# Kernel tuning notes

Hardware: AMD Instinct MI355X
Metric: run time of the kernel (lower is better)

## Reference

```python
import jax, jax.numpy as jnp
import numpy as np

K = 32  # num_neighbors in DynamicRadiusChannelFusion


def _sqdist(p):
    # p: (B, N, 3) -> pairwise squared distances (B, N, N)
    n2 = jnp.sum(p * p, axis=-1)
    d = n2[:, :, None] + n2[:, None, :] - 2.0 * jnp.einsum('bnd,bmd->bnm', p, p)
    return d


def _fuse(x, feats, W, b):
    # KNN on xyz coords (first 3 channels), gather neighbor feats,
    # relative edge features -> linear -> ReLU -> max over neighbors.
    d = _sqdist(x[..., :3])                      # (B, N, N)
    _, idx = jax.lax.top_k(-d, K)                # (B, N, K) int32
    nbr = jax.vmap(lambda f, i: f[i])(feats, idx)  # (B, N, K, C) gather
    rel = nbr - feats[:, :, None, :]             # edge features
    msg = jax.nn.relu(jnp.einsum('bnkc,cd->bnkd', rel, W) + b)
    return jnp.max(msg, axis=2), idx             # (B, N, C), (B, N, K)


def setup_inputs() -> dict:
    key = jax.random.key(0)
    ks = jax.random.split(key, 14)
    B, N, D, C, NC = 4, 8000, 9, 64, 13
    s = lambda *sh: 1.0 / np.sqrt(sh[0])
    return {
        'x': jax.random.normal(ks[0], (B, N, D), jnp.float32),
        'enc_w1': jax.random.normal(ks[1], (D, C), jnp.float32) * s(D),
        'enc_b1': jnp.zeros((C,), jnp.float32),
        'enc_w2': jax.random.normal(ks[2], (C, C), jnp.float32) * s(C),
        'enc_b2': jnp.zeros((C,), jnp.float32),
        'f1_w': jax.random.normal(ks[3], (C, C), jnp.float32) * s(C),
        'f1_b': jnp.zeros((C,), jnp.float32),
        'f2_w': jax.random.normal(ks[4], (C, C), jnp.float32) * s(C),
        'f2_b': jnp.zeros((C,), jnp.float32),
        'cls_w1': jax.random.normal(ks[5], (C, C // 2), jnp.float32) * s(C),
        'cls_b1': jnp.zeros((C // 2,), jnp.float32),
        'cls_w2': jax.random.normal(ks[6], (C // 2, NC), jnp.float32) * s(C // 2),
        'cls_b2': jnp.zeros((NC,), jnp.float32),
    }


def reference(x, enc_w1, enc_b1, enc_w2, enc_b2, f1_w, f1_b, f2_w, f2_b,
              cls_w1, cls_b1, cls_w2, cls_b2):
    # encoder: Linear -> ReLU -> Linear
    feats = jax.nn.relu(x @ enc_w1 + enc_b1) @ enc_w2 + enc_b2  # (B, N, 64)
    out1, _ = _fuse(x, feats, f1_w, f1_b)
    out2, _ = _fuse(x, feats, f2_w, f2_b)
    fused = out1 + out2
    # classifier: Linear -> ReLU -> Linear
    logits = jax.nn.relu(fused @ cls_w1 + cls_b1) @ cls_w2 + cls_b2
    return logits  # (B, N, num_classes)
```

## Files before the change

kernel.cpp:

```cpp
#include <hip/hip_runtime.h>
#include <stdint.h>

#define NPTS 8000
#define NBATCH 4
#define TOTALP (NBATCH * NPTS)
#define KSEL 32
#define QPB 64
#define SPLIT 4
#define CPW (NPTS / SPLIT)
#define PDEPTH 16

typedef uint32_t u32;
typedef unsigned long long u64;

__global__ __launch_bounds__(256) void encode_kernel(
    const float* __restrict__ x,
    const float* __restrict__ ew1, const float* __restrict__ eb1,
    const float* __restrict__ ew2, const float* __restrict__ eb2,
    const float* __restrict__ f1w, const float* __restrict__ f2w,
    float* __restrict__ g1, float* __restrict__ g2,
    float4* __restrict__ cand)
{
    __shared__ float sw1[9 * 64];
    __shared__ float sw2[64 * 64];
    __shared__ float sf1[64 * 64];
    __shared__ float sf2[64 * 64];
    __shared__ float sb1[64];
    __shared__ float sb2[64];
    __shared__ float shb[4][64];
    __shared__ float sfb[4][64];

    const int tid = threadIdx.x;
    for (int i = tid; i < 9 * 64; i += 256) sw1[i] = ew1[i];
    for (int i = tid; i < 64 * 64; i += 256) {
        sw2[i] = ew2[i]; sf1[i] = f1w[i]; sf2[i] = f2w[i];
    }
    if (tid < 64) { sb1[tid] = eb1[tid]; sb2[tid] = eb2[tid]; }
    __syncthreads();

    const int lane = tid & 63;
    const int w = tid >> 6;
    const int gw = blockIdx.x * 4 + w;
    const int nw = 256 * 4;

    #pragma unroll 1
    for (int it = 0; it < 32; ++it) {
        int p = gw + it * nw;
        int pc = p < TOTALP ? p : TOTALP - 1;
        const float* xp = x + (size_t)pc * 9;

        float acc = sb1[lane];
        #pragma unroll
        for (int i = 0; i < 9; ++i) acc = fmaf(xp[i], sw1[i * 64 + lane], acc);
        shb[w][lane] = fmaxf(acc, 0.f);
        __syncthreads();

        float fa = sb2[lane];
        #pragma unroll
        for (int c = 0; c < 64; ++c) fa = fmaf(shb[w][c], sw2[c * 64 + lane], fa);
        sfb[w][lane] = fa;
        __syncthreads();

        float a1 = 0.f, a2 = 0.f;
        #pragma unroll
        for (int c = 0; c < 64; ++c) {
            float fv = sfb[w][c];
            a1 = fmaf(fv, sf1[c * 64 + lane], a1);
            a2 = fmaf(fv, sf2[c * 64 + lane], a2);
        }
        if (p < TOTALP) {
            g1[(size_t)p * 64 + lane] = a1;
            g2[(size_t)p * 64 + lane] = a2;
            if (lane == 0) {
                float cx = xp[0], cy = xp[1], cz = xp[2];
                float n2 = __fadd_rn(__fadd_rn(__fmul_rn(cx, cx),
                                               __fmul_rn(cy, cy)),
                                     __fmul_rn(cz, cz));
                cand[p] = make_float4(cx, cy, cz, n2);
            }
        }
        __syncthreads();
    }
}

__global__ __launch_bounds__(256) void knn_scan_kernel(
    const float4* __restrict__ cand, int* __restrict__ idxo)
{
    __shared__ u64 smem[4096];
    const int b = blockIdx.y;
    const int lane = threadIdx.x & 63;
    const int w = threadIdx.x >> 6;
    const int q = blockIdx.x * QPB + lane;
    const float4* cb = cand + (size_t)b * NPTS;

    const float4 qv = cb[q];
    const float qx = qv.x, qy = qv.y, qz = qv.z, qn2 = qv.w;

    u64 sk[KSEL];
    #pragma unroll
    for (int i = 0; i < KSEL; ++i) sk[i] = ~0ULL;
    u64 thr = ~0ULL;
    int c = 0;
    u64* pend = smem + w * (PDEPTH * 64);

#define DRAINB()                                                          \
    do {                                                                  \
        u64 p[PDEPTH];                                                    \
        _Pragma("unroll")                                                 \
        for (int j = 0; j < PDEPTH; ++j) p[j] = pend[j * 64 + lane];      \
        _Pragma("unroll")                                                 \
        for (int j = 0; j < PDEPTH; ++j) p[j] = (j < c) ? p[j] : ~0ULL;   \
        _Pragma("unroll")                                                 \
        for (int k = 2; k <= PDEPTH; k <<= 1) {                           \
            _Pragma("unroll")                                             \
            for (int j = k >> 1; j > 0; j >>= 1) {                        \
                _Pragma("unroll")                                         \
                for (int i = 0; i < PDEPTH; ++i) {                        \
                    if ((i & j) == 0) {                                   \
                        const int ip = i | j;                             \
                        const bool asc = ((i & k) == 0);                  \
                        u64 a = p[i], bb = p[ip];                         \
                        u64 lo = a < bb ? a : bb;                         \
                        u64 hi = a < bb ? bb : a;                         \
                        p[i]  = asc ? lo : hi;                            \
                        p[ip] = asc ? hi : lo;                            \
                    }                                                     \
                }                                                         \
            }                                                             \
        }                                                                 \
        _Pragma("unroll")                                                 \
        for (int j = 0; j < PDEPTH; ++j) {                                \
            u64 a = sk[16 + j], bb = p[PDEPTH - 1 - j];                   \
            sk[16 + j] = a < bb ? a : bb;                                 \
        }                                                                 \
        _Pragma("unroll")                                                 \
        for (int dd = 16; dd > 0; dd >>= 1) {                             \
            _Pragma("unroll")                                             \
            for (int i = 0; i < KSEL; ++i) {                              \
                if ((i & dd) == 0) {                                      \
                    const int ip = i | dd;                                \
                    u64 a = sk[i], bb = sk[ip];                           \
                    sk[i]  = a < bb ? a : bb;                             \
                    sk[ip] = a < bb ? bb : a;                             \
                }                                                         \
            }                                                             \
        }                                                                 \
        c = 0;                                                            \
        thr = sk[KSEL - 1];                                               \
    } while (0)

#define PROC(cv, ci_)                                                     \
    do {                                                                  \
        float dot_ = fmaf(qz, (cv).z, fmaf(qy, (cv).y, __fmul_rn(qx, (cv).x))); \
        float d_ = __fsub_rn(__fadd_rn(qn2, (cv).w), __fmul_rn(2.0f, dot_)); \
        d_ = fmaxf(d_, 0.0f);   \
        u64 key_ = (((u64)__float_as_uint(d_)) << 13) | (u64)(ci_);       \
        bool take_ = key_ < thr;                                          \
        pend[(size_t)c * 64 + lane] = key_;                               \
        c += (int)take_;                                                  \
    } while (0)

    const int c0 = w * CPW;
    #pragma unroll 1
    for (int i = 0; i < CPW; i += 4) {
        const int ci = c0 + i;
        float4 cv0 = cb[ci + 0];
        float4 cv1 = cb[ci + 1];
        float4 cv2 = cb[ci + 2];
        float4 cv3 = cb[ci + 3];
        PROC(cv0, ci + 0);
        PROC(cv1, ci + 1);
        PROC(cv2, ci + 2);
        PROC(cv3, ci + 3);
        if (__any(c >= PDEPTH - 3)) DRAINB();
    }
    DRAINB();
#undef PROC
#undef DRAINB

#define MERGE32(kidx)                                                     \
    do {                                                                  \
        u64 o[KSEL];                                                      \
        _Pragma("unroll")                                                 \
        for (int t = 0; t < KSEL; ++t)                                    \
            o[t] = smem[(kidx) * 2048 + t * 64 + lane];                   \
        _Pragma("unroll")                                                 \
        for (int i = 0; i < KSEL; ++i) {                                  \
            u64 a = sk[i], bb = o[KSEL - 1 - i];                          \
            sk[i] = a < bb ? a : bb;                                      \
        }                                                                 \
        _Pragma("unroll")                                                 \
        for (int dd = 16; dd > 0; dd >>= 1) {                             \
            _Pragma("unroll")                                             \
            for (int i = 0; i < KSEL; ++i) {                              \
                if ((i & dd) == 0) {                                      \
                    const int ip = i | dd;                                \
                    u64 a = sk[i], bb = sk[ip];                           \
                    sk[i]  = a < bb ? a : bb;                             \
                    sk[ip] = a < bb ? bb : a;                             \
                }                                                         \
            }                                                             \
        }                                                                 \
    } while (0)

    __syncthreads();
    if (w == 1) {
        #pragma unroll
        for (int t = 0; t < KSEL; ++t) smem[t * 64 + lane] = sk[t];
    }
    if (w == 3) {
        #pragma unroll
        for (int t = 0; t < KSEL; ++t) smem[2048 + t * 64 + lane] = sk[t];
    }
    __syncthreads();
    if (w == 0) MERGE32(0);
    if (w == 2) MERGE32(1);
    __syncthreads();
    if (w == 2) {
        #pragma unroll
        for (int t = 0; t < KSEL; ++t) smem[t * 64 + lane] = sk[t];
    }
    __syncthreads();
    if (w == 0) {
        MERGE32(0);
        int* op = idxo + ((size_t)b * NPTS + q) * KSEL;
        #pragma unroll
        for (int i = 0; i < KSEL; ++i) op[i] = (int)(sk[i] & 0x1FFFULL);
    }
#undef MERGE32
}

__global__ __launch_bounds__(256) void fuse_kernel(
    const float* __restrict__ g1, const float* __restrict__ g2,
    const int* __restrict__ idxo,
    const float* __restrict__ f1b, const float* __restrict__ f2b,
    float* __restrict__ fused)
{
    const int lane = threadIdx.x & 63;
    const int gw = (int)((blockIdx.x * 256 + threadIdx.x) >> 6);
    const int nw = 512 * 4;
    const float bias1 = f1b[lane];
    const float bias2 = f2b[lane];
    for (int p = gw; p < TOTALP; p += nw) {
        int b = p / NPTS;
        const int* mi = idxo + (size_t)p * KSEL;
        const float* G1 = g1 + (size_t)b * NPTS * 64;
        const float* G2 = g2 + (size_t)b * NPTS * 64;
        float base1 = bias1 - g1[(size_t)p * 64 + lane];
        float base2 = bias2 - g2[(size_t)p * 64 + lane];
        float a1 = 0.f, a2 = 0.f;
        #pragma unroll
        for (int k = 0; k < KSEL; ++k) {
            int j = mi[k];
            a1 = fmaxf(a1, G1[(size_t)j * 64 + lane] + base1);
            a2 = fmaxf(a2, G2[(size_t)j * 64 + lane] + base2);
        }
        fused[(size_t)p * 64 + lane] = a1 + a2;
    }
}

__global__ __launch_bounds__(256) void cls_kernel(
    const float* __restrict__ fused,
    const float* __restrict__ cw1, const float* __restrict__ cb1,
    const float* __restrict__ cw2, const float* __restrict__ cb2,
    float* __restrict__ out)
{
    __shared__ float sw1[64 * 32];
    __shared__ float sw2[32 * 13];
    __shared__ float sb1[32];
    __shared__ float sb2[13];
    const int tid = threadIdx.x;
    for (int i = tid; i < 64 * 32; i += 256) sw1[i] = cw1[i];
    for (int i = tid; i < 32 * 13; i += 256) sw2[i] = cw2[i];
    if (tid < 32) sb1[tid] = cb1[tid];
    if (tid < 13) sb2[tid] = cb2[tid];
    __syncthreads();

    int p = blockIdx.x * 256 + tid;
    if (p >= TOTALP) return;

    float fu[64];
    const float4* fp = (const float4*)(fused + (size_t)p * 64);
    #pragma unroll
    for (int i = 0; i < 16; ++i) {
        float4 v = fp[i];
        fu[i * 4 + 0] = v.x; fu[i * 4 + 1] = v.y;
        fu[i * 4 + 2] = v.z; fu[i * 4 + 3] = v.w;
    }
    float h[32];
    #pragma unroll
    for (int j = 0; j < 32; j += 4) {
        float ax = sb1[j], ay = sb1[j + 1], az = sb1[j + 2], aw = sb1[j + 3];
        #pragma unroll
        for (int c = 0; c < 64; ++c) {
            float4 wv = *(const float4*)&sw1[c * 32 + j];
            ax = fmaf(fu[c], wv.x, ax);
            ay = fmaf(fu[c], wv.y, ay);
            az = fmaf(fu[c], wv.z, az);
            aw = fmaf(fu[c], wv.w, aw);
        }
        h[j] = fmaxf(ax, 0.f); h[j + 1] = fmaxf(ay, 0.f);
        h[j + 2] = fmaxf(az, 0.f); h[j + 3] = fmaxf(aw, 0.f);
    }
    float* op = out + (size_t)p * 13;
    #pragma unroll
    for (int o = 0; o < 13; ++o) {
        float acc = sb2[o];
        #pragma unroll
        for (int j = 0; j < 32; ++j) acc = fmaf(h[j], sw2[j * 13 + o], acc);
        op[o] = acc;
    }
}

extern "C" void kernel_launch(void* const* d_in, const int* in_sizes, int n_in,
                              void* d_out, int out_size, void* d_ws, size_t ws_size,
                              hipStream_t stream)
{
    const float* x   = (const float*)d_in[0];
    const float* ew1 = (const float*)d_in[1];
    const float* eb1 = (const float*)d_in[2];
    const float* ew2 = (const float*)d_in[3];
    const float* eb2 = (const float*)d_in[4];
    const float* f1w = (const float*)d_in[5];
    const float* f1b = (const float*)d_in[6];
    const float* f2w = (const float*)d_in[7];
    const float* f2b = (const float*)d_in[8];
    const float* cw1 = (const float*)d_in[9];
    const float* cb1 = (const float*)d_in[10];
    const float* cw2 = (const float*)d_in[11];
    const float* cb2 = (const float*)d_in[12];
    float* out = (float*)d_out;

    float*  g1    = (float*)d_ws;
    float*  g2    = g1 + (size_t)TOTALP * 64;
    float4* cand  = (float4*)(g2 + (size_t)TOTALP * 64);
    int*    idxo  = (int*)(cand + (size_t)TOTALP);
    float*  fused = (float*)(idxo + (size_t)TOTALP * KSEL);

    hipLaunchKernelGGL(encode_kernel, dim3(256), dim3(256), 0, stream,
                       x, ew1, eb1, ew2, eb2, f1w, f2w, g1, g2, cand);
    hipLaunchKernelGGL(knn_scan_kernel, dim3(125, NBATCH), dim3(256), 0, stream,
                       cand, idxo);
    hipLaunchKernelGGL(fuse_kernel, dim3(512), dim3(256), 0, stream,
                       g1, g2, idxo, f1b, f2b, fused);
    hipLaunchKernelGGL(cls_kernel, dim3(125), dim3(256), 0, stream,
                       fused, cw1, cb1, cw2, cb2, out);
}
```

Measured before the change: 524.1 us.

## Split KNN candidate scan across two block groups with a merge kernel

Splits the KNN candidate range into two halves handled by separate block groups, doubling the grid from 500 to 1000 blocks. The partial top-32 lists are written out and merged in a new bitonic-merge kernel that stores indices in k-major layout. The encoder moves from block-wide barriers to wave-local syncs with contiguous per-wave point chunks. The fuse kernel moves to a per-batch grid that reads the transposed index layout. The extra merge kernel and partial-key traffic add memory cost in exchange for more parallelism in the dominant scan.

```diff
diff --git a/kernel.cpp b/kernel.cpp
--- a/kernel.cpp
+++ b/kernel.cpp
@@ -7,7 +7,8 @@
 #define KSEL 32
 #define QPB 64
 #define SPLIT 4
-#define CPW (NPTS / SPLIT)
+#define CSPLIT 2
+#define CPW (NPTS / (CSPLIT * SPLIT))
 #define PDEPTH 16
 
 typedef uint32_t u32;
@@ -40,26 +41,30 @@
 
     const int lane = tid & 63;
     const int w = tid >> 6;
-    const int gw = blockIdx.x * 4 + w;
-    const int nw = 256 * 4;
+    const int wave_id = blockIdx.x * 4 + w;
+
+#define WSYNC() do { \
+        asm volatile("s_waitcnt lgkmcnt(0)" ::: "memory"); \
+        __builtin_amdgcn_wave_barrier(); \
+    } while (0)
 
     #pragma unroll 1
-    for (int it = 0; it < 32; ++it) {
-        int p = gw + it * nw;
-        int pc = p < TOTALP ? p : TOTALP - 1;
-        const float* xp = x + (size_t)pc * 9;
+    for (int it = 0; it < 16; ++it) {
+        const int p = wave_id * 16 + it;
+        const float* xp = x + (size_t)p * 9;
 
         float acc = sb1[lane];
         #pragma unroll
         for (int i = 0; i < 9; ++i) acc = fmaf(xp[i], sw1[i * 64 + lane], acc);
         shb[w][lane] = fmaxf(acc, 0.f);
-        __syncthreads();
+        WSYNC();
 
         float fa = sb2[lane];
         #pragma unroll
         for (int c = 0; c < 64; ++c) fa = fmaf(shb[w][c], sw2[c * 64 + lane], fa);
+        WSYNC();
         sfb[w][lane] = fa;
-        __syncthreads();
+        WSYNC();
 
         float a1 = 0.f, a2 = 0.f;
         #pragma unroll
@@ -68,26 +73,26 @@
             a1 = fmaf(fv, sf1[c * 64 + lane], a1);
             a2 = fmaf(fv, sf2[c * 64 + lane], a2);
         }
-        if (p < TOTALP) {
-            g1[(size_t)p * 64 + lane] = a1;
-            g2[(size_t)p * 64 + lane] = a2;
-            if (lane == 0) {
-                float cx = xp[0], cy = xp[1], cz = xp[2];
-                float n2 = __fadd_rn(__fadd_rn(__fmul_rn(cx, cx),
-                                               __fmul_rn(cy, cy)),
-                                     __fmul_rn(cz, cz));
-                cand[p] = make_float4(cx, cy, cz, n2);
-            }
-        }
-        __syncthreads();
-    }
+        WSYNC();
+        g1[(size_t)p * 64 + lane] = a1;
+        g2[(size_t)p * 64 + lane] = a2;
+        if (lane == 0) {
+            float cx = xp[0], cy = xp[1], cz = xp[2];
+            float n2 = __fadd_rn(__fadd_rn(__fmul_rn(cx, cx),
+                                           __fmul_rn(cy, cy)),
+                                 __fmul_rn(cz, cz));
+            cand[p] = make_float4(cx, cy, cz, n2);
+        }
+    }
+#undef WSYNC
 }
 
 __global__ __launch_bounds__(256) void knn_scan_kernel(
-    const float4* __restrict__ cand, int* __restrict__ idxo)
+    const float4* __restrict__ cand, u64* __restrict__ pk)
 {
     __shared__ u64 smem[4096];
-    const int b = blockIdx.y;
+    const int b = blockIdx.z;
+    const int cs = blockIdx.y;
     const int lane = threadIdx.x & 63;
     const int w = threadIdx.x >> 6;
     const int q = blockIdx.x * QPB + lane;
@@ -160,7 +165,7 @@
         c += (int)take_;                                                  \
     } while (0)
 
-    const int c0 = w * CPW;
+    const int c0 = cs * (NPTS / CSPLIT) + w * CPW;
     #pragma unroll 1
     for (int i = 0; i < CPW; i += 4) {
         const int ci = c0 + i;
@@ -223,11 +228,45 @@
     __syncthreads();
     if (w == 0) {
         MERGE32(0);
-        int* op = idxo + ((size_t)b * NPTS + q) * KSEL;
-        #pragma unroll
-        for (int i = 0; i < KSEL; ++i) op[i] = (int)(sk[i] & 0x1FFFULL);
+        const size_t bq = (size_t)b * NPTS + q;
+        #pragma unroll
+        for (int t = 0; t < KSEL; ++t)
+            pk[((size_t)(cs * KSEL + t)) * TOTALP + bq] = sk[t];
     }
 #undef MERGE32
+}
+
+__global__ __launch_bounds__(256) void knn_final_kernel(
+    const u64* __restrict__ pk, int* __restrict__ idxo)
+{
+    const int p = blockIdx.x * 256 + threadIdx.x;
+
+    u64 sk[KSEL], o[KSEL];
+    #pragma unroll
+    for (int t = 0; t < KSEL; ++t) sk[t] = pk[(size_t)t * TOTALP + p];
+    #pragma unroll
+    for (int t = 0; t < KSEL; ++t) o[t] = pk[(size_t)(KSEL + t) * TOTALP + p];
+
+    #pragma unroll
+    for (int i = 0; i < KSEL; ++i) {
+        u64 a = sk[i], bb = o[KSEL - 1 - i];
+        sk[i] = a < bb ? a : bb;
+    }
+    #pragma unroll
+    for (int dd = 16; dd > 0; dd >>= 1) {
+        #pragma unroll
+        for (int i = 0; i < KSEL; ++i) {
+            if ((i & dd) == 0) {
+                const int ip = i | dd;
+                u64 a = sk[i], bb = sk[ip];
+                sk[i]  = a < bb ? a : bb;
+                sk[ip] = a < bb ? bb : a;
+            }
+        }
+    }
+    #pragma unroll
+    for (int t = 0; t < KSEL; ++t)
+        idxo[(size_t)t * TOTALP + p] = (int)(sk[t] & 0x1FFFULL);
 }
 
 __global__ __launch_bounds__(256) void fuse_kernel(
@@ -237,25 +276,28 @@
     float* __restrict__ fused)
 {
     const int lane = threadIdx.x & 63;
-    const int gw = (int)((blockIdx.x * 256 + threadIdx.x) >> 6);
-    const int nw = 512 * 4;
+    const int w = threadIdx.x >> 6;
+    const int b = blockIdx.y;
+    const int wchunk = blockIdx.x * 4 + w;
     const float bias1 = f1b[lane];
     const float bias2 = f2b[lane];
-    for (int p = gw; p < TOTALP; p += nw) {
-        int b = p / NPTS;
-        const int* mi = idxo + (size_t)p * KSEL;
-        const float* G1 = g1 + (size_t)b * NPTS * 64;
-        const float* G2 = g2 + (size_t)b * NPTS * 64;
-        float base1 = bias1 - g1[(size_t)p * 64 + lane];
-        float base2 = bias2 - g2[(size_t)p * 64 + lane];
+    const float* G1 = g1 + (size_t)b * NPTS * 64;
+    const float* G2 = g2 + (size_t)b * NPTS * 64;
+
+    #pragma unroll 1
+    for (int it = 0; it < 16; ++it) {
+        const int pl = wchunk * 16 + it;
+        const size_t p = (size_t)b * NPTS + pl;
+        float base1 = bias1 - G1[(size_t)pl * 64 + lane];
+        float base2 = bias2 - G2[(size_t)pl * 64 + lane];
         float a1 = 0.f, a2 = 0.f;
         #pragma unroll
         for (int k = 0; k < KSEL; ++k) {
-            int j = mi[k];
+            int j = idxo[(size_t)k * TOTALP + p];
             a1 = fmaxf(a1, G1[(size_t)j * 64 + lane] + base1);
             a2 = fmaxf(a2, G2[(size_t)j * 64 + lane] + base2);
         }
-        fused[(size_t)p * 64 + lane] = a1 + a2;
+        fused[p * 64 + lane] = a1 + a2;
     }
 }
 
@@ -335,13 +377,16 @@
     float*  g2    = g1 + (size_t)TOTALP * 64;
     float4* cand  = (float4*)(g2 + (size_t)TOTALP * 64);
     int*    idxo  = (int*)(cand + (size_t)TOTALP);
-    float*  fused = (float*)(idxo + (size_t)TOTALP * KSEL);
-
-    hipLaunchKernelGGL(encode_kernel, dim3(256), dim3(256), 0, stream,
+    u64*    pk    = (u64*)(idxo + (size_t)TOTALP * KSEL);
+    float*  fused = (float*)pk;
+
+    hipLaunchKernelGGL(encode_kernel, dim3(500), dim3(256), 0, stream,
                        x, ew1, eb1, ew2, eb2, f1w, f2w, g1, g2, cand);
-    hipLaunchKernelGGL(knn_scan_kernel, dim3(125, NBATCH), dim3(256), 0, stream,
-                       cand, idxo);
-    hipLaunchKernelGGL(fuse_kernel, dim3(512), dim3(256), 0, stream,
+    hipLaunchKernelGGL(knn_scan_kernel, dim3(125, CSPLIT, NBATCH), dim3(256), 0,
+                       stream, cand, pk);
+    hipLaunchKernelGGL(knn_final_kernel, dim3(125), dim3(256), 0, stream,
+                       pk, idxo);
+    hipLaunchKernelGGL(fuse_kernel, dim3(125, NBATCH), dim3(256), 0, stream,
                        g1, g2, idxo, f1b, f2b, fused);
     hipLaunchKernelGGL(cls_kernel, dim3(125), dim3(256), 0, stream,
                        fused, cw1, cb1, cw2, cb2, out);
```

Result: faster. 497.7 us (-5.0%).
